# Kernel optimization log

Hardware: AMD Instinct MI355X
Metric: run time of the kernel (lower is better)

## Reference

```python
import jax, jax.numpy as jnp
import numpy as np

CODEBOOK_SIZE = 8192
LATENT_DIM = 12
EPS = 1e-12


def conv_s4(x, w, b):
    # Conv1d with kernel=stride=4 (non-overlapping): x (N,C,L), w (O,C,4) torch layout
    n, c, L = x.shape
    xr = x.reshape(n, c, L // 4, 4)
    return jnp.einsum('nclk,ock->nol', xr, w) + b[None, :, None]


def deconv_s4(x, w, b):
    # ConvTranspose1d with kernel=stride=4: x (N,C,L), w (C,O,4) torch layout
    n, c, L = x.shape
    y = jnp.einsum('ncl,cok->nolk', x, w).reshape(n, w.shape[1], L * 4)
    return y + b[None, :, None]


def setup_inputs() -> dict:
    key = jax.random.key(0)
    ks = jax.random.split(key, 16)
    s = 0.1
    inp = {
        'x': jax.random.normal(ks[0], (2048, 1, 1024), dtype=jnp.float32),
        'w1': jax.random.normal(ks[1], (16, 1, 4), dtype=jnp.float32) * s,
        'b1': jnp.zeros((16,), jnp.float32),
        'w2': jax.random.normal(ks[2], (32, 16, 4), dtype=jnp.float32) * s,
        'b2': jnp.zeros((32,), jnp.float32),
        'w3': jax.random.normal(ks[3], (LATENT_DIM, 32, 4), dtype=jnp.float32) * s,
        'b3': jnp.zeros((LATENT_DIM,), jnp.float32),
        'd1w': jax.random.normal(ks[4], (LATENT_DIM, 32, 4), dtype=jnp.float32) * s,
        'd1b': jnp.zeros((32,), jnp.float32),
        'd2w': jax.random.normal(ks[5], (32, 16, 4), dtype=jnp.float32) * s,
        'd2b': jnp.zeros((16,), jnp.float32),
        'd3w': jax.random.normal(ks[6], (16, 1, 4), dtype=jnp.float32) * s,
        'd3b': jnp.zeros((1,), jnp.float32),
    }
    cb = jax.random.normal(ks[7], (CODEBOOK_SIZE, LATENT_DIM), dtype=jnp.float32)
    inp['codebook'] = cb / jnp.maximum(jnp.linalg.norm(cb, axis=1, keepdims=True), EPS)
    return inp


def reference(x, w1, b1, w2, b2, w3, b3, codebook, d1w, d1b, d2w, d2b, d3w, d3b):
    # encoder (push)
    h = jax.nn.relu(conv_s4(x, w1, b1))
    h = jax.nn.relu(conv_s4(h, w2, b2))
    continuous = conv_s4(h, w3, b3)                      # (N, 12, 16)
    # L2 normalize along channel dim (F.normalize p=2 dim=1)
    continuous = continuous / jnp.maximum(
        jnp.linalg.norm(continuous, axis=1, keepdims=True), EPS)
    # flatten to points: (N*16, 12)
    flat = continuous.transpose(0, 2, 1).reshape(-1, LATENT_DIM)
    # nearest codebook entry: argmin of squared euclidean dist (|x|^2 term constant per row)
    d2 = jnp.sum(codebook * codebook, axis=1)[None, :] - 2.0 * (flat @ codebook.T)
    idx = jnp.argmin(d2, axis=1)                          # (N*16,)
    quantized = codebook[idx].reshape(-1, 16, LATENT_DIM).transpose(0, 2, 1)  # (N,12,16)
    # straight-through estimator
    quantized_ste = continuous + jax.lax.stop_gradient(quantized - continuous)
    # decoder (pop)
    g = jax.nn.relu(deconv_s4(quantized_ste, d1w, d1b))
    g = jax.nn.relu(deconv_s4(g, d2w, d2b))
    recon = deconv_s4(g, d3w, d3b)                        # (N, 1, 1024)
    return recon, continuous, quantized
```

## Files before the change

### kernel.cpp

```cpp
#include <hip/hip_runtime.h>
#include <math.h>

#define WSB_Q64   0u
#define WSB_QZ    3145728u
#define WSB_KEYS  4718592u
#define WSB_CCH   4980736u
#define WSB_W1D   5046272u
#define WSB_W2D   5046784u
#define WSB_W3D   5063168u
#define WSB_B1D   5075456u
#define WSB_B2D   5075584u
#define WSB_B3D   5075840u
#define WSB_D1R   5075936u
#define WSB_D2R   5082080u
#define WSB_D3R   5090272u
#define WSB_CB16  5090528u
#define WSB_Q16   5352672u
#define DELTA 0.003f
#define SCALE46 70368744177664.0
#define WCAP 512

typedef _Float16 half8 __attribute__((ext_vector_type(8)));
typedef float f32x16 __attribute__((ext_vector_type(16)));

__device__ __forceinline__ float relu(float v) { return v > 0.f ? v : 0.f; }

__device__ __forceinline__ unsigned okey(float s) {
  unsigned u = __float_as_uint(s);
  return u ^ ((u & 0x80000000u) ? 0xFFFFFFFFu : 0x80000000u);
}
__device__ __forceinline__ float unokey(unsigned k) {
  unsigned u = k ^ ((k & 0x80000000u) ? 0x80000000u : 0xFFFFFFFFu);
  return __uint_as_float(u);
}

__global__ __launch_bounds__(256) void k_prep(
    const float* __restrict__ w1, const float* __restrict__ b1,
    const float* __restrict__ w2, const float* __restrict__ b2,
    const float* __restrict__ w3, const float* __restrict__ b3,
    const float* __restrict__ cbk, const float* __restrict__ d1w,
    const float* __restrict__ d2w, const float* __restrict__ d3w,
    unsigned long long* __restrict__ keys, unsigned* __restrict__ qmax,
    double* __restrict__ cch,
    double* __restrict__ w1d, double* __restrict__ w2d,
    double* __restrict__ w3d, double* __restrict__ b1d,
    double* __restrict__ b2d, double* __restrict__ b3d,
    float* __restrict__ d1r, float* __restrict__ d2r,
    float* __restrict__ d3r, _Float16* __restrict__ cb16) {
  int gid = blockIdx.x * 256 + threadIdx.x;
  keys[gid] = 0ull;
  qmax[gid] = 0u;
  if (gid < 8192) {
    double s = 0.0;
    half8 lo, hi;
#pragma unroll
    for (int d = 0; d < 12; d++) {
      float cf = cbk[gid * 12 + d];
      double c = (double)cf;
      s = fma(c, c, s);
      if (d < 8) lo[d] = (_Float16)cf; else hi[d - 8] = (_Float16)cf;
    }
#pragma unroll
    for (int d = 4; d < 8; d++) hi[d] = (_Float16)0.f;
    cch[gid] = 0.5 * s;
    int tile = gid >> 5, col = gid & 31;
    *(half8*)(cb16 + (size_t)(tile * 64 + col) * 8) = lo;
    *(half8*)(cb16 + (size_t)(tile * 64 + 32 + col) * 8) = hi;
  }
  if (blockIdx.x == 0) {
    int t = threadIdx.x;
    for (int i = t; i < 64; i += 256) w1d[i] = (double)w1[i];
    for (int i = t; i < 16; i += 256) b1d[i] = (double)b1[i];
    for (int i = t; i < 32; i += 256) b2d[i] = (double)b2[i];
    for (int i = t; i < 12; i += 256) b3d[i] = (double)b3[i];
    for (int i = t; i < 2048; i += 256) {
      int k = i >> 9, o = (i >> 4) & 31, c = i & 15;
      w2d[i] = (double)w2[o * 64 + c * 4 + k];
    }
    for (int i = t; i < 1536; i += 256) {
      int q = i / 384, r = i % 384, j = r >> 5, o = r & 31;
      w3d[i] = (double)w3[j * 128 + o * 4 + q];
    }
    for (int i = t; i < 1536; i += 256) {
      int p = i / 384, r = i % 384, o = r / 12, c = r % 12;
      d1r[i] = d1w[c * 128 + o * 4 + p];
    }
    for (int i = t; i < 2048; i += 256) {
      int k = i >> 9, o = (i >> 5) & 15, c = i & 31;
      d2r[i] = d2w[c * 64 + o * 4 + k];
    }
    for (int i = t; i < 64; i += 256) {
      int k = i >> 4, c = i & 15;
      d3r[i] = d3w[c * 4 + k];
    }
  }
}

__global__ __launch_bounds__(512, 2) void k_enc(
    const float* __restrict__ x, const double* __restrict__ w1d,
    const double* __restrict__ w2d, const double* __restrict__ w3d,
    const double* __restrict__ b1d, const double* __restrict__ b2d,
    const double* __restrict__ b3d, float* __restrict__ cont_out,
    double* __restrict__ q64out, _Float16* __restrict__ q16out) {
  __shared__ double w2s[2048];
  __shared__ double w3s[1536];
  __shared__ double w1s[64];
  __shared__ double b1s[16], b2s[32], b3s[12];
  __shared__ double red[2][8][64][12];

  int t = threadIdx.x;
  for (int i = t; i < 2048; i += 512) w2s[i] = w2d[i];
  for (int i = t; i < 1536; i += 512) w3s[i] = w3d[i];
  if (t < 64) w1s[t] = w1d[t];
  else if (t >= 64 && t < 80) b1s[t - 64] = b1d[t - 64];
  else if (t >= 80 && t < 112) b2s[t - 80] = b2d[t - 80];
  else if (t >= 112 && t < 124) b3s[t - 112] = b3d[t - 112];
  __syncthreads();

  int w = t >> 6, lane = t & 63;
  int qq = w & 3, oh = w >> 2;
  int winA = blockIdx.x * 64 + lane;
  int winB = winA + 16384;
  const float* xbA = x + (winA >> 4) * 1024 + (winA & 15) * 64 + qq * 16;
  const float* xbB = x + (winB >> 4) * 1024 + (winB & 15) * 64 + qq * 16;

  double h2A[16], h2B[16];
#pragma unroll
  for (int o = 0; o < 16; o++) { h2A[o] = b2s[oh * 16 + o]; h2B[o] = h2A[o]; }

#pragma unroll 1
  for (int k = 0; k < 4; k++) {
    float4 xvA = *reinterpret_cast<const float4*>(xbA + 4 * k);
    float4 xvB = *reinterpret_cast<const float4*>(xbB + 4 * k);
    double xA0 = (double)xvA.x, xA1 = (double)xvA.y;
    double xA2 = (double)xvA.z, xA3 = (double)xvA.w;
    double xB0 = (double)xvB.x, xB1 = (double)xvB.y;
    double xB2 = (double)xvB.z, xB3 = (double)xvB.w;
    double h1A[16], h1B[16];
#pragma unroll
    for (int c = 0; c < 16; c++) {
      double2 wa = *(const double2*)(w1s + 4 * c);
      double2 wb = *(const double2*)(w1s + 4 * c + 2);
      double bb = b1s[c];
      double sA = bb, sB = bb;
      sA = fma(xA0, wa.x, sA); sB = fma(xB0, wa.x, sB);
      sA = fma(xA1, wa.y, sA); sB = fma(xB1, wa.y, sB);
      sA = fma(xA2, wb.x, sA); sB = fma(xB2, wb.x, sB);
      sA = fma(xA3, wb.y, sA); sB = fma(xB3, wb.y, sB);
      h1A[c] = sA > 0.0 ? sA : 0.0;
      h1B[c] = sB > 0.0 ? sB : 0.0;
    }
    const double* w2k = w2s + k * 512 + oh * 256;
#pragma unroll
    for (int o = 0; o < 16; o++) {
      const double* wp = w2k + o * 16;
      double sA = h2A[o], sB = h2B[o];
#pragma unroll
      for (int c = 0; c < 16; c += 2) {
        double2 wv = *(const double2*)(wp + c);
        sA = fma(h1A[c], wv.x, sA); sA = fma(h1A[c + 1], wv.y, sA);
        sB = fma(h1B[c], wv.x, sB); sB = fma(h1B[c + 1], wv.y, sB);
      }
      h2A[o] = sA; h2B[o] = sB;
    }
  }
#pragma unroll
  for (int o = 0; o < 16; o++) {
    h2A[o] = h2A[o] > 0.0 ? h2A[o] : 0.0;
    h2B[o] = h2B[o] > 0.0 ? h2B[o] : 0.0;
  }

  const double* w3q = w3s + qq * 384 + oh * 16;
#pragma unroll
  for (int j = 0; j < 12; j++) {
    const double* wp = w3q + j * 32;
    double sA = 0.0, sB = 0.0;
#pragma unroll
    for (int o = 0; o < 16; o += 2) {
      double2 wv = *(const double2*)(wp + o);
      sA = fma(h2A[o], wv.x, sA); sA = fma(h2A[o + 1], wv.y, sA);
      sB = fma(h2B[o], wv.x, sB); sB = fma(h2B[o + 1], wv.y, sB);
    }
    red[0][w][lane][j] = sA;
    red[1][w][lane][j] = sB;
  }
  __syncthreads();

  if (w < 2) {
    int set = w;
    int win = blockIdx.x * 64 + lane + set * 16384;
    int n = win >> 4, l = win & 15;
    double cont[12], ss = 0.0;
#pragma unroll
    for (int j = 0; j < 12; j++) {
      double v = b3s[j] +
          (((red[set][0][lane][j] + red[set][1][lane][j]) +
            (red[set][2][lane][j] + red[set][3][lane][j])) +
           ((red[set][4][lane][j] + red[set][5][lane][j]) +
            (red[set][6][lane][j] + red[set][7][lane][j])));
      cont[j] = v;
      ss = fma(v, v, ss);
    }
    double nrm = sqrt(ss);
    if (nrm < 1e-12) nrm = 1e-12;
    half8 lo, hi;
#pragma unroll
    for (int j = 0; j < 12; j++) {
      double qv = cont[j] / nrm;
      float qf = (float)qv;
      cont_out[n * 192 + j * 16 + l] = qf;
      q64out[(size_t)win * 12 + j] = qv;
      if (j < 8) lo[j] = (_Float16)qf; else hi[j - 8] = (_Float16)qf;
    }
#pragma unroll
    for (int j = 4; j < 8; j++) hi[j] = (_Float16)0.f;
    *(half8*)(q16out + (size_t)win * 16) = lo;
    *(half8*)(q16out + (size_t)win * 16 + 8) = hi;
  }
}

__global__ __launch_bounds__(256, 2) void k_vq1(
    const _Float16* __restrict__ q16, const _Float16* __restrict__ cbf,
    unsigned* __restrict__ qmax) {
  int t = threadIdx.x;
  int w = t >> 6, lane = t & 63;
  int half = lane >> 5, col = lane & 31;
  int qg = blockIdx.x >> 3;
  int cq = blockIdx.x & 7;
  int qbase = qg * 128 + w * 32;
  const _Float16* bp = cbf + (size_t)cq * 32 * 64 * 8;

  half8 a = *(const half8*)(q16 + (size_t)(qbase + col) * 16 + half * 8);
  f32x16 z = {0.f, 0.f, 0.f, 0.f, 0.f, 0.f, 0.f, 0.f,
              0.f, 0.f, 0.f, 0.f, 0.f, 0.f, 0.f, 0.f};

  half8 b0 = *(const half8*)(bp + (0 * 64 + lane) * 8);
  half8 b1 = *(const half8*)(bp + (1 * 64 + lane) * 8);
  half8 b2 = *(const half8*)(bp + (2 * 64 + lane) * 8);
  half8 b3 = *(const half8*)(bp + (3 * 64 + lane) * 8);

  float mx[16];
#pragma unroll
  for (int r = 0; r < 16; r++) mx[r] = -3.f;

  f32x16 dp = __builtin_amdgcn_mfma_f32_32x32x16_f16(a, b0, z, 0, 0, 0);
  b0 = b1; b1 = b2; b2 = b3;
  b3 = *(const half8*)(bp + (4 * 64 + lane) * 8);

#pragma unroll 4
  for (int tt = 1; tt < 32; tt++) {
    f32x16 d = __builtin_amdgcn_mfma_f32_32x32x16_f16(a, b0, z, 0, 0, 0);
    b0 = b1; b1 = b2; b2 = b3;
    if (tt + 4 < 32) b3 = *(const half8*)(bp + ((tt + 4) * 64 + lane) * 8);
#pragma unroll
    for (int r = 0; r < 16; r++) mx[r] = fmaxf(mx[r], dp[r]);
    dp = d;
  }
#pragma unroll
  for (int r = 0; r < 16; r++) mx[r] = fmaxf(mx[r], dp[r]);

#pragma unroll
  for (int m = 1; m <= 16; m <<= 1) {
#pragma unroll
    for (int r = 0; r < 16; r++) mx[r] = fmaxf(mx[r], __shfl_xor(mx[r], m));
  }
#pragma unroll
  for (int r = 0; r < 16; r++) {
    if (col == r) {
      unsigned row = (r & 3) + 8 * (r >> 2) + 4 * half;
      atomicMax(&qmax[qbase + row], okey(mx[r]));
    }
  }
}

__global__ __launch_bounds__(256, 2) void k_vq2(
    const _Float16* __restrict__ q16, const _Float16* __restrict__ cbf,
    const unsigned* __restrict__ qmax, const double* __restrict__ q64,
    const float* __restrict__ cbk, const double* __restrict__ cchalf,
    unsigned long long* __restrict__ keys) {
  __shared__ unsigned wlist[4][WCAP];
  __shared__ int wcnt[4];
  int t = threadIdx.x;
  int w = t >> 6, lane = t & 63;
  int half = lane >> 5, col = lane & 31;
  if (lane == 0) wcnt[w] = 0;
  int qg = blockIdx.x >> 3;
  int cq = blockIdx.x & 7;
  int qbase = qg * 128 + w * 32;
  int cbase = cq * 1024;
  const _Float16* bp = cbf + (size_t)cq * 32 * 64 * 8;

  half8 a = *(const half8*)(q16 + (size_t)(qbase + col) * 16 + half * 8);
  f32x16 z = {0.f, 0.f, 0.f, 0.f, 0.f, 0.f, 0.f, 0.f,
              0.f, 0.f, 0.f, 0.f, 0.f, 0.f, 0.f, 0.f};

  float thr[16];
#pragma unroll
  for (int r = 0; r < 16; r++) {
    unsigned row = (r & 3) + 8 * (r >> 2) + 4 * half;
    thr[r] = unokey(qmax[qbase + row]) - DELTA;
  }

  half8 b0 = *(const half8*)(bp + (0 * 64 + lane) * 8);
  half8 b1 = *(const half8*)(bp + (1 * 64 + lane) * 8);
  half8 b2 = *(const half8*)(bp + (2 * 64 + lane) * 8);
  half8 b3 = *(const half8*)(bp + (3 * 64 + lane) * 8);

#define CONSUME(dv, ttv)                                                      \
  {                                                                           \
    _Pragma("unroll") for (int r = 0; r < 16; r++) {                          \
      if (dv[r] >= thr[r]) {                                                  \
        int slot = atomicAdd(&wcnt[w], 1);                                    \
        unsigned row = (r & 3) + 8 * (r >> 2) + 4 * half;                     \
        unsigned enc = ((unsigned)(qbase + row) << 13) |                      \
                       (unsigned)(cbase + (ttv)*32 + col);                    \
        if (slot < WCAP) wlist[w][slot] = enc;                                \
      }                                                                       \
    }                                                                         \
  }

  f32x16 dp = __builtin_amdgcn_mfma_f32_32x32x16_f16(a, b0, z, 0, 0, 0);
  b0 = b1; b1 = b2; b2 = b3;
  b3 = *(const half8*)(bp + (4 * 64 + lane) * 8);

#pragma unroll 4
  for (int tt = 1; tt < 32; tt++) {
    f32x16 d = __builtin_amdgcn_mfma_f32_32x32x16_f16(a, b0, z, 0, 0, 0);
    b0 = b1; b1 = b2; b2 = b3;
    if (tt + 4 < 32) b3 = *(const half8*)(bp + ((tt + 4) * 64 + lane) * 8);
    CONSUME(dp, tt - 1);
    dp = d;
  }
  CONSUME(dp, 31);
#undef CONSUME

  int n = wcnt[w];
  if (n > WCAP) n = WCAP;
  for (int i = lane; i < n; i += 64) {
    unsigned e = wlist[w][i];
    int q = e >> 13, c = e & 8191;
    const double* qp = q64 + (size_t)q * 12;
    const float* cp = cbk + c * 12;
    double s = 0.0;
#pragma unroll
    for (int dd = 0; dd < 12; dd++) s = fma(qp[dd], (double)cp[dd], s);
    unsigned long long ek =
        (unsigned long long)((s - cchalf[c] + 2.0) * SCALE46);
    atomicMax(&keys[q], (ek << 16) | (unsigned)(8191 - c));
  }
}

__global__ __launch_bounds__(256) void k_unpack(
    const unsigned long long* __restrict__ keys,
    const float* __restrict__ codebook, float* __restrict__ quant_out,
    float* __restrict__ qz) {
  int q = blockIdx.x * 256 + threadIdx.x;
  int gidx = 8191 - (int)(keys[q] & 0xFFFFull);
  int n = q >> 4, l = q & 15;
  const float* cp = codebook + gidx * 12;
#pragma unroll
  for (int c = 0; c < 12; c++) {
    float v = cp[c];
    quant_out[n * 192 + c * 16 + l] = v;
    qz[q * 12 + c] = v;
  }
}

__global__ __launch_bounds__(256) void k_dec(
    const float* __restrict__ qz, const float* __restrict__ d1r,
    const float* __restrict__ d2r, const float* __restrict__ d3r,
    const float* __restrict__ d1b, const float* __restrict__ d2b,
    const float* __restrict__ d3b, float* __restrict__ rec) {
  int t = threadIdx.x;
  int p2 = t >> 6, lane = t & 63;
  int win = blockIdx.x * 64 + lane;
  const float4* qp = reinterpret_cast<const float4*>(qz + win * 12);
  float4 q0 = qp[0], q1 = qp[1], q2 = qp[2];

  const float* d1p = d1r + p2 * 384;
  float y1[32];
#pragma unroll
  for (int o = 0; o < 32; o++) {
    const float4* wp = reinterpret_cast<const float4*>(d1p + o * 12);
    float4 a0 = wp[0], a1 = wp[1], a2 = wp[2];
    float s = d1b[o];
    s = fmaf(q0.x, a0.x, s); s = fmaf(q0.y, a0.y, s);
    s = fmaf(q0.z, a0.z, s); s = fmaf(q0.w, a0.w, s);
    s = fmaf(q1.x, a1.x, s); s = fmaf(q1.y, a1.y, s);
    s = fmaf(q1.z, a1.z, s); s = fmaf(q1.w, a1.w, s);
    s = fmaf(q2.x, a2.x, s); s = fmaf(q2.y, a2.y, s);
    s = fmaf(q2.z, a2.z, s); s = fmaf(q2.w, a2.w, s);
    y1[o] = relu(s);
  }

  float d3bias = d3b[0];
#pragma unroll 1
  for (int k = 0; k < 4; k++) {
    const float* d2k = d2r + k * 512;
    float y2[16];
#pragma unroll
    for (int o = 0; o < 16; o++) {
      const float4* wp = reinterpret_cast<const float4*>(d2k + o * 32);
      float s = d2b[o];
#pragma unroll
      for (int g = 0; g < 8; g++) {
        float4 a = wp[g];
        s = fmaf(y1[4 * g + 0], a.x, s); s = fmaf(y1[4 * g + 1], a.y, s);
        s = fmaf(y1[4 * g + 2], a.z, s); s = fmaf(y1[4 * g + 3], a.w, s);
      }
      y2[o] = relu(s);
    }
    float ov[4];
#pragma unroll
    for (int kk = 0; kk < 4; kk++) {
      const float4* wp = reinterpret_cast<const float4*>(d3r + kk * 16);
      float s = d3bias;
#pragma unroll
      for (int g = 0; g < 4; g++) {
        float4 a = wp[g];
        s = fmaf(y2[4 * g + 0], a.x, s); s = fmaf(y2[4 * g + 1], a.y, s);
        s = fmaf(y2[4 * g + 2], a.z, s); s = fmaf(y2[4 * g + 3], a.w, s);
      }
      ov[kk] = s;
    }
    *reinterpret_cast<float4*>(rec + win * 64 + p2 * 16 + k * 4) =
        make_float4(ov[0], ov[1], ov[2], ov[3]);
  }
}

extern "C" void kernel_launch(void* const* d_in, const int* in_sizes, int n_in,
                              void* d_out, int out_size, void* d_ws,
                              size_t ws_size, hipStream_t stream) {
  const float* x  = (const float*)d_in[0];
  const float* w1 = (const float*)d_in[1];
  const float* b1 = (const float*)d_in[2];
  const float* w2 = (const float*)d_in[3];
  const float* b2 = (const float*)d_in[4];
  const float* w3 = (const float*)d_in[5];
  const float* b3 = (const float*)d_in[6];
  int cb_idx = (in_sizes[13] == 98304) ? 13 : 7;
  int dbase = (cb_idx == 13) ? 7 : 8;
  const float* cbk = (const float*)d_in[cb_idx];
  const float* d1w = (const float*)d_in[dbase + 0];
  const float* d1b = (const float*)d_in[dbase + 1];
  const float* d2w = (const float*)d_in[dbase + 2];
  const float* d2b = (const float*)d_in[dbase + 3];
  const float* d3w = (const float*)d_in[dbase + 4];
  const float* d3b = (const float*)d_in[dbase + 5];

  float* out = (float*)d_out;
  float* rec = out;
  float* cont_out = out + 2097152;
  float* quant_out = out + 2490368;

  char* wsb = (char*)d_ws;
  double* q64 = (double*)(wsb + WSB_Q64);
  float* qz = (float*)(wsb + WSB_QZ);
  unsigned* qmax = (unsigned*)(wsb + WSB_QZ);
  unsigned long long* keys = (unsigned long long*)(wsb + WSB_KEYS);
  double* cch = (double*)(wsb + WSB_CCH);
  double* w1d = (double*)(wsb + WSB_W1D);
  double* w2d = (double*)(wsb + WSB_W2D);
  double* w3d = (double*)(wsb + WSB_W3D);
  double* b1d = (double*)(wsb + WSB_B1D);
  double* b2d = (double*)(wsb + WSB_B2D);
  double* b3d = (double*)(wsb + WSB_B3D);
  float* d1r = (float*)(wsb + WSB_D1R);
  float* d2r = (float*)(wsb + WSB_D2R);
  float* d3r = (float*)(wsb + WSB_D3R);
  _Float16* cb16 = (_Float16*)(wsb + WSB_CB16);
  _Float16* q16 = (_Float16*)(wsb + WSB_Q16);

  k_prep<<<128, 256, 0, stream>>>(w1, b1, w2, b2, w3, b3, cbk, d1w, d2w, d3w,
                                  keys, qmax, cch, w1d, w2d, w3d, b1d, b2d,
                                  b3d, d1r, d2r, d3r, cb16);
  k_enc<<<256, 512, 0, stream>>>(x, w1d, w2d, w3d, b1d, b2d, b3d, cont_out,
                                 q64, q16);
  k_vq1<<<2048, 256, 0, stream>>>(q16, cb16, qmax);
  k_vq2<<<2048, 256, 0, stream>>>(q16, cb16, qmax, q64, cbk, cch, keys);
  k_unpack<<<128, 256, 0, stream>>>(keys, cbk, quant_out, qz);
  k_dec<<<512, 256, 0, stream>>>(qz, d1r, d2r, d3r, d1b, d2b, d3b, rec);
}
```

Before: 134.2 us.

## Fuse unpack into decoder, move buffer zeroing into consumer kernels, raise occupancy

```diff
diff --git a/kernel.cpp b/kernel.cpp
--- a/kernel.cpp
+++ b/kernel.cpp
@@ -40,7 +40,6 @@
     const float* __restrict__ w3, const float* __restrict__ b3,
     const float* __restrict__ cbk, const float* __restrict__ d1w,
     const float* __restrict__ d2w, const float* __restrict__ d3w,
-    unsigned long long* __restrict__ keys, unsigned* __restrict__ qmax,
     double* __restrict__ cch,
     double* __restrict__ w1d, double* __restrict__ w2d,
     double* __restrict__ w3d, double* __restrict__ b1d,
@@ -48,8 +47,6 @@
     float* __restrict__ d1r, float* __restrict__ d2r,
     float* __restrict__ d3r, _Float16* __restrict__ cb16) {
   int gid = blockIdx.x * 256 + threadIdx.x;
-  keys[gid] = 0ull;
-  qmax[gid] = 0u;
   if (gid < 8192) {
     double s = 0.0;
     half8 lo, hi;
@@ -101,7 +98,8 @@
     const double* __restrict__ w2d, const double* __restrict__ w3d,
     const double* __restrict__ b1d, const double* __restrict__ b2d,
     const double* __restrict__ b3d, float* __restrict__ cont_out,
-    double* __restrict__ q64out, _Float16* __restrict__ q16out) {
+    double* __restrict__ q64out, _Float16* __restrict__ q16out,
+    unsigned* __restrict__ qmax) {
   __shared__ double w2s[2048];
   __shared__ double w3s[1536];
   __shared__ double w1s[64];
@@ -109,6 +107,9 @@
   __shared__ double red[2][8][64][12];
 
   int t = threadIdx.x;
+  int gid0 = blockIdx.x * 512 + t;
+  if (gid0 < 32768) qmax[gid0] = 0u;
+
   for (int i = t; i < 2048; i += 512) w2s[i] = w2d[i];
   for (int i = t; i < 1536; i += 512) w3s[i] = w3d[i];
   if (t < 64) w1s[t] = w1d[t];
@@ -219,14 +220,15 @@
   }
 }
 
-__global__ __launch_bounds__(256, 2) void k_vq1(
+__global__ __launch_bounds__(256, 4) void k_vq1(
     const _Float16* __restrict__ q16, const _Float16* __restrict__ cbf,
-    unsigned* __restrict__ qmax) {
+    unsigned* __restrict__ qmax, unsigned long long* __restrict__ keys) {
   int t = threadIdx.x;
   int w = t >> 6, lane = t & 63;
   int half = lane >> 5, col = lane & 31;
   int qg = blockIdx.x >> 3;
   int cq = blockIdx.x & 7;
+  if (cq == 0 && t < 128) keys[qg * 128 + t] = 0ull;
   int qbase = qg * 128 + w * 32;
   const _Float16* bp = cbf + (size_t)cq * 32 * 64 * 8;
 
@@ -273,7 +275,7 @@
   }
 }
 
-__global__ __launch_bounds__(256, 2) void k_vq2(
+__global__ __launch_bounds__(256, 3) void k_vq2(
     const _Float16* __restrict__ q16, const _Float16* __restrict__ cbf,
     const unsigned* __restrict__ qmax, const double* __restrict__ q64,
     const float* __restrict__ cbk, const double* __restrict__ cchalf,
@@ -350,32 +352,29 @@
   }
 }
 
-__global__ __launch_bounds__(256) void k_unpack(
+__global__ __launch_bounds__(256) void k_dec(
     const unsigned long long* __restrict__ keys,
-    const float* __restrict__ codebook, float* __restrict__ quant_out,
-    float* __restrict__ qz) {
-  int q = blockIdx.x * 256 + threadIdx.x;
-  int gidx = 8191 - (int)(keys[q] & 0xFFFFull);
-  int n = q >> 4, l = q & 15;
-  const float* cp = codebook + gidx * 12;
-#pragma unroll
-  for (int c = 0; c < 12; c++) {
-    float v = cp[c];
-    quant_out[n * 192 + c * 16 + l] = v;
-    qz[q * 12 + c] = v;
-  }
-}
-
-__global__ __launch_bounds__(256) void k_dec(
-    const float* __restrict__ qz, const float* __restrict__ d1r,
+    const float* __restrict__ cbk, const float* __restrict__ d1r,
     const float* __restrict__ d2r, const float* __restrict__ d3r,
     const float* __restrict__ d1b, const float* __restrict__ d2b,
-    const float* __restrict__ d3b, float* __restrict__ rec) {
+    const float* __restrict__ d3b, float* __restrict__ quant_out,
+    float* __restrict__ rec) {
   int t = threadIdx.x;
   int p2 = t >> 6, lane = t & 63;
   int win = blockIdx.x * 64 + lane;
-  const float4* qp = reinterpret_cast<const float4*>(qz + win * 12);
-  float4 q0 = qp[0], q1 = qp[1], q2 = qp[2];
+  int gidx = 8191 - (int)(keys[win] & 0xFFFFull);
+  const float* cp = cbk + gidx * 12;
+  float4 q0 = *(const float4*)(cp);
+  float4 q1 = *(const float4*)(cp + 4);
+  float4 q2 = *(const float4*)(cp + 8);
+
+  if (p2 == 0) {
+    int n = win >> 4, l = win & 15;
+    float* qo = quant_out + n * 192 + l;
+    qo[0] = q0.x;  qo[16] = q0.y;  qo[32] = q0.z;  qo[48] = q0.w;
+    qo[64] = q1.x; qo[80] = q1.y;  qo[96] = q1.z;  qo[112] = q1.w;
+    qo[128] = q2.x; qo[144] = q2.y; qo[160] = q2.z; qo[176] = q2.w;
+  }
 
   const float* d1p = d1r + p2 * 384;
   float y1[32];
@@ -455,7 +454,6 @@
 
   char* wsb = (char*)d_ws;
   double* q64 = (double*)(wsb + WSB_Q64);
-  float* qz = (float*)(wsb + WSB_QZ);
   unsigned* qmax = (unsigned*)(wsb + WSB_QZ);
   unsigned long long* keys = (unsigned long long*)(wsb + WSB_KEYS);
   double* cch = (double*)(wsb + WSB_CCH);
@@ -471,13 +469,13 @@
   _Float16* cb16 = (_Float16*)(wsb + WSB_CB16);
   _Float16* q16 = (_Float16*)(wsb + WSB_Q16);
 
-  k_prep<<<128, 256, 0, stream>>>(w1, b1, w2, b2, w3, b3, cbk, d1w, d2w, d3w,
-                                  keys, qmax, cch, w1d, w2d, w3d, b1d, b2d,
-                                  b3d, d1r, d2r, d3r, cb16);
+  k_prep<<<32, 256, 0, stream>>>(w1, b1, w2, b2, w3, b3, cbk, d1w, d2w, d3w,
+                                 cch, w1d, w2d, w3d, b1d, b2d, b3d,
+                                 d1r, d2r, d3r, cb16);
   k_enc<<<256, 512, 0, stream>>>(x, w1d, w2d, w3d, b1d, b2d, b3d, cont_out,
-                                 q64, q16);
-  k_vq1<<<2048, 256, 0, stream>>>(q16, cb16, qmax);
+                                 q64, q16, qmax);
+  k_vq1<<<2048, 256, 0, stream>>>(q16, cb16, qmax, keys);
   k_vq2<<<2048, 256, 0, stream>>>(q16, cb16, qmax, q64, cbk, cch, keys);
-  k_unpack<<<128, 256, 0, stream>>>(keys, cbk, quant_out, qz);
-  k_dec<<<512, 256, 0, stream>>>(qz, d1r, d2r, d3r, d1b, d2b, d3b, rec);
-}
+  k_dec<<<512, 256, 0, stream>>>(keys, cbk, d1r, d2r, d3r, d1b, d2b, d3b,
+                                 quant_out, rec);
+}
```

Result: no change. 131.8 us (-1.8%).
